# Optimization experiments

Measured on AMD Instinct MI355X. Metric: run time of the kernel, lower is better.

The kernel has to match this reference:

```python
import jax, jax.numpy as jnp
import numpy as np

NUM_VARS = 10
HID = 256
INP = 4
B = 32
T = 64

_adj = np.ones((NUM_VARS, NUM_VARS)) - np.eye(NUM_VARS)
SEND, RECV = np.where(_adj)          # each [E], E = num_vars*(num_vars-1) = 90
E = len(SEND)
_e2n = np.zeros((NUM_VARS, E), dtype=np.float32)
_e2n[RECV, np.arange(E)] = 1.0       # encode_onehot(recv).T -> [num_vars, E]
E2N = jnp.asarray(_e2n)
SEND_J = jnp.asarray(SEND)
RECV_J = jnp.asarray(RECV)


def _mlp_block(x, w1, b1, w2, b2, gamma, beta):
    # RefNRIMLP: elu(fc1) -> (dropout p=0) -> elu(fc2) -> batchnorm over view(-1, H)
    h = jax.nn.elu(x @ w1 + b1)
    h = jax.nn.elu(h @ w2 + b2)
    mu = h.mean(axis=(0, 1, 2), keepdims=True)
    var = h.var(axis=(0, 1, 2), keepdims=True)
    return gamma * (h - mu) * jax.lax.rsqrt(var + 1e-5) + beta


def setup_inputs() -> dict:
    key = jax.random.key(0)
    ks = jax.random.split(key, 12)

    def xavier(k, fi, fo):
        return jax.random.normal(k, (fi, fo), jnp.float32) * np.sqrt(2.0 / (fi + fo))

    d = {
        "x": jax.random.normal(ks[0], (B, T, NUM_VARS, INP), jnp.float32),
        # mlp1: inp -> hid -> hid
        "w1a": xavier(ks[1], INP, HID), "b1a": jnp.full((HID,), 0.1),
        "w1b": xavier(ks[2], HID, HID), "b1b": jnp.full((HID,), 0.1),
        "g1": jnp.ones((HID,)), "be1": jnp.zeros((HID,)),
        # mlp2: 2*hid -> hid -> hid
        "w2a": xavier(ks[3], 2 * HID, HID), "b2a": jnp.full((HID,), 0.1),
        "w2b": xavier(ks[4], HID, HID), "b2b": jnp.full((HID,), 0.1),
        "g2": jnp.ones((HID,)), "be2": jnp.zeros((HID,)),
        # mlp3: hid -> hid -> hid
        "w3a": xavier(ks[5], HID, HID), "b3a": jnp.full((HID,), 0.1),
        "w3b": xavier(ks[6], HID, HID), "b3b": jnp.full((HID,), 0.1),
        "g3": jnp.ones((HID,)), "be3": jnp.zeros((HID,)),
        # output heads
        "wo1": xavier(ks[7], HID, HID), "bo1": jnp.full((HID,), 0.1),
        "wo2": xavier(ks[8], HID, 1), "bo2": jnp.full((1,), 0.1),
    }
    return d


def reference(x, w1a, b1a, w1b, b1b, g1, be1,
              w2a, b2a, w2b, b2b, g2, be2,
              w3a, b3a, w3b, b3b, g3, be3,
              wo1, bo1, wo2, bo2):
    # x: [B, T, N, INP] -> transpose(2,1): [B, N, T, INP]
    h = jnp.transpose(x, (0, 2, 1, 3))
    h = _mlp_block(h, w1a, b1a, w1b, b1b, g1, be1)            # [B, N, T, H]
    # node2edge: gather senders/receivers along node dim, concat on features
    e = jnp.concatenate([h[:, SEND_J], h[:, RECV_J]], axis=-1)  # [B, E, T, 2H]
    e = _mlp_block(e, w2a, b2a, w2b, b2b, g2, be2)            # [B, E, T, H]
    # edge2node: incidence matmul over edge dim, normalize by in-degree
    n = jnp.einsum('ve,betH->bvtH', E2N, e) / (NUM_VARS - 1)   # [B, N, T, H]
    n = _mlp_block(n, w3a, b3a, w3b, b3b, g3, be3)
    n = jax.nn.relu(n) @ wo1 + bo1
    n = jax.nn.relu(n) @ wo2 + bo2                             # [B, N, T, 1]
    out = jnp.transpose(n, (0, 2, 1, 3)).mean(axis=-1)         # [B, T, N]
    return out
```

## Files before the change

kernel.cpp:

```cpp
#include <hip/hip_runtime.h>
#include <hip/hip_bf16.h>
#include <cstdint>

#define DI __device__ __forceinline__

typedef short bf16x8 __attribute__((ext_vector_type(8)));
typedef float f32x4 __attribute__((ext_vector_type(4)));
typedef unsigned short u16;
typedef unsigned short u16x8 __attribute__((ext_vector_type(8)));

static constexpr int NV = 10, NE = 90, TT = 64;
static constexpr int R1 = 20480;
static constexpr int R2 = 184320;

DI float bf2f(u16 u) { union { unsigned int i; float f; } x; x.i = ((unsigned int)u) << 16; return x.f; }
DI u16 f2bf(float f) { unsigned int u = __float_as_uint(f); return (u16)((u + 0x7FFF + ((u >> 16) & 1)) >> 16); }
DI float elu(float v) { return v > 0.f ? v : __expf(v) - 1.f; }

#define GLL(srcp, dstp) __builtin_amdgcn_global_load_lds( \
    (const __attribute__((address_space(1))) unsigned int*)(srcp), \
    (__attribute__((address_space(3))) unsigned int*)(dstp), 16, 0, 0)

__global__ __launch_bounds__(256) void pack5(
    const float* __restrict__ s0, u16* __restrict__ d0,
    const float* __restrict__ s1, u16* __restrict__ d1,
    const float* __restrict__ s2, u16* __restrict__ d2,
    const float* __restrict__ s3, u16* __restrict__ d3,
    const float* __restrict__ s4, u16* __restrict__ d4) {
    const float* s; u16* d;
    switch (blockIdx.y) {
        case 0: s = s0; d = d0; break;
        case 1: s = s1; d = d1; break;
        case 2: s = s2; d = d2; break;
        case 3: s = s3; d = d3; break;
        default: s = s4; d = d4; break;
    }
    int tid = threadIdx.x;
    int bn = blockIdx.x >> 3, kt = blockIdx.x & 7;
#pragma unroll
    for (int p = 0; p < 2; ++p) {
        int n = bn * 128 + p * 64 + (tid >> 2);
        int k = kt * 32 + (tid & 3) * 8;
        u16x8 pk;
#pragma unroll
        for (int e = 0; e < 8; ++e) pk[e] = f2bf(s[(size_t)(k + e) * 256 + n]);
        *(u16x8*)(d + ((size_t)((bn * 8 + kt) * 2 + p)) * 2048 + (size_t)tid * 8) = pk;
    }
}

__global__ __launch_bounds__(256) void pack_w2a(const float* __restrict__ w2a,
                                                const float* __restrict__ scsh1,
                                                u16* __restrict__ d) {
    int tid = threadIdx.x;
    int bn = blockIdx.x >> 4, kt = blockIdx.x & 15;
#pragma unroll
    for (int p = 0; p < 2; ++p) {
        int n = bn * 128 + p * 64 + (tid >> 2);
        int k = kt * 32 + (tid & 3) * 8;
        u16x8 pk;
#pragma unroll
        for (int e = 0; e < 8; ++e)
            pk[e] = f2bf(scsh1[(k + e) & 255] * w2a[(size_t)(k + e) * 256 + n]);
        *(u16x8*)(d + ((size_t)((bn * 16 + kt) * 2 + p)) * 2048 + (size_t)tid * 8) = pk;
    }
}

__global__ void zero_stats(float* p, int n) {
    int i = blockIdx.x * 256 + threadIdx.x;
    if (i < n) p[i] = 0.f;
}

__global__ void conv_wo2(const float* __restrict__ src, u16* __restrict__ dst) {
    dst[threadIdx.x] = f2bf(src[threadIdx.x]);
}

__global__ __launch_bounds__(256) void fold_b2a(const float* __restrict__ w2a,
                                                const float* __restrict__ scsh1,
                                                const float* __restrict__ b2a,
                                                float* __restrict__ b2aF) {
    __shared__ float red[256];
    int n = blockIdx.x, tid = threadIdx.x;
    float sc = scsh1[256 + tid];
    float s = sc * w2a[tid * 256 + n] + sc * w2a[(tid + 256) * 256 + n];
    red[tid] = s;
    __syncthreads();
    for (int off2 = 128; off2 > 0; off2 >>= 1) {
        if (tid < off2) red[tid] += red[tid + off2];
        __syncthreads();
    }
    if (tid == 0) b2aF[n] = red[0] + b2a[n];
}

__global__ void stats_final(const float* __restrict__ sums, const float* __restrict__ g,
                            const float* __restrict__ be, float invR, float* __restrict__ scsh) {
    int c = threadIdx.x;
    float mu = sums[c] * invR;
    float var = sums[256 + c] * invR - mu * mu;
    float rs = rsqrtf(var + 1e-5f);
    float sc = g[c] * rs;
    scsh[c] = sc;
    scsh[256 + c] = be[c] - mu * sc;
}

__global__ __launch_bounds__(256) void mlp1_fc1(const float* __restrict__ x,
                                                const float* __restrict__ w1a,
                                                const float* __restrict__ b1a,
                                                u16* __restrict__ ha) {
    int tid = threadIdx.x;
    int row = blockIdx.x * 8 + (tid >> 5);
    int ch8 = (tid & 31) * 8;
    int b = row / (NV * TT);
    int v = (row >> 6) % NV;
    int t = row & 63;
    const float* xp = x + ((size_t)(b * TT + t) * NV + v) * 4;
    float x0 = xp[0], x1 = xp[1], x2 = xp[2], x3 = xp[3];
    u16x8 pack;
#pragma unroll
    for (int e = 0; e < 8; ++e) {
        int c = ch8 + e;
        float acc = b1a[c] + x0 * w1a[c] + x1 * w1a[256 + c] + x2 * w1a[512 + c] + x3 * w1a[768 + c];
        pack[e] = f2bf(elu(acc));
    }
    *(u16x8*)(ha + (size_t)row * 256 + ch8) = pack;
}

template <bool GATHER, int ACT, bool STATS, int SWZ>
__global__ __launch_bounds__(256) void gemm_kernel(const u16* __restrict__ A,
                                                   const u16* __restrict__ Wt,
                                                   const float* __restrict__ bias,
                                                   u16* __restrict__ out,
                                                   int K,
                                                   float* __restrict__ stats) {
    __shared__ u16 As[3][128 * 32];
    __shared__ u16 Bs[3][128 * 32];
    const int tid = threadIdx.x;
    const int lane = tid & 63, wid = tid >> 6;

    int bm, bn;
    {
        int bid = blockIdx.x;
        int xcd = bid & 7, slot = bid >> 3;
        if constexpr (SWZ == 1) {
            int batch = xcd + 8 * (slot / 90);
            int j = slot % 90;
            bn = j & 1;
            bm = batch * 45 + (j >> 1);
        } else {
            bn = slot & 1;
            bm = xcd + 8 * (slot >> 1);
        }
    }
    const int m0 = bm * 128, n0 = bn * 128;
    const int wm = wid >> 1, wn = wid & 1;

    const int srow = tid >> 2;
    const int scol8 = (tid & 3) * 8;

    size_t abase[2], sb[2], rb[2];
    if constexpr (GATHER) {
#pragma unroll
        for (int p = 0; p < 2; ++p) {
            int m = m0 + srow + p * 64;
            int t = m & 63;
            int be = m >> 6;
            int e = be % NE;
            int b = be / NE;
            int s = e / 9;
            int kk = e - s * 9;
            int r = kk + (kk >= s ? 1 : 0);
            sb[p] = ((size_t)((b * NV + s) * TT + t)) * 256;
            rb[p] = ((size_t)((b * NV + r) * TT + t)) * 256;
        }
    } else {
#pragma unroll
        for (int p = 0; p < 2; ++p) abase[p] = (size_t)(m0 + srow + p * 64) * K;
    }
    const int NT = K >> 5;
    const size_t bnbase = (size_t)bn * NT * 4096;

    f32x4 acc[4][4];
#pragma unroll
    for (int i = 0; i < 4; ++i)
#pragma unroll
        for (int j = 0; j < 4; ++j) acc[i][j] = (f32x4)0.f;

    const int lrow = lane & 15;
    const int lk8 = (lane >> 4) * 8;

    auto stage = [&](int bf, int k0) {
        const size_t btile = bnbase + (size_t)(k0 >> 5) * 4096 + (size_t)tid * 8;
#pragma unroll
        for (int p = 0; p < 2; ++p) {
            const u16* asrc;
            if constexpr (GATHER) {
                int f = k0 + scol8;
                asrc = A + (f < 256 ? sb[p] + f : rb[p] + (f - 256));
            } else {
                asrc = A + abase[p] + k0 + scol8;
            }
            GLL(asrc, &As[bf][(p * 256 + wid * 64) * 8]);
            GLL(Wt + btile + p * 2048, &Bs[bf][(p * 256 + wid * 64) * 8]);
        }
    };

    stage(0, 0);
    stage(1, 32);
    for (int kt = 0; kt < NT; ++kt) {
        if (kt + 1 < NT) {
            asm volatile("s_waitcnt vmcnt(4)" ::: "memory");
        } else {
            asm volatile("s_waitcnt vmcnt(0)" ::: "memory");
        }
        __builtin_amdgcn_s_barrier();
        if (kt + 2 < NT) stage((kt + 2) % 3, (kt + 2) * 32);
        __builtin_amdgcn_sched_barrier(0);
        const int buf = kt % 3;
        bf16x8 a[4], b[4];
#pragma unroll
        for (int i = 0; i < 4; ++i)
            a[i] = *(const bf16x8*)&As[buf][(wm * 64 + i * 16 + lrow) * 32 + lk8];
#pragma unroll
        for (int j = 0; j < 4; ++j)
            b[j] = *(const bf16x8*)&Bs[buf][(wn * 64 + j * 16 + lrow) * 32 + lk8];
#pragma unroll
        for (int i = 0; i < 4; ++i)
#pragma unroll
            for (int j = 0; j < 4; ++j)
                acc[i][j] = __builtin_amdgcn_mfma_f32_16x16x32_bf16(a[i], b[j], acc[i][j], 0, 0, 0);
    }

    float bv[4], sv[4], qv[4];
#pragma unroll
    for (int j = 0; j < 4; ++j) {
        bv[j] = bias[n0 + wn * 64 + j * 16 + lrow];
        if constexpr (STATS) { sv[j] = 0.f; qv[j] = 0.f; }
    }
#pragma unroll
    for (int i = 0; i < 4; ++i) {
#pragma unroll
        for (int j = 0; j < 4; ++j) {
            int col = n0 + wn * 64 + j * 16 + lrow;
#pragma unroll
            for (int r = 0; r < 4; ++r) {
                int row = m0 + wm * 64 + i * 16 + (lane >> 4) * 4 + r;
                float v = acc[i][j][r] + bv[j];
                v = (ACT == 1) ? elu(v) : (v > 0.f ? v : 0.f);
                if constexpr (STATS) { sv[j] += v; qv[j] += v * v; }
                out[(size_t)row * 256 + col] = f2bf(v);
            }
        }
    }
    if constexpr (STATS) {
#pragma unroll
        for (int j = 0; j < 4; ++j) {
            float s = sv[j], q_ = qv[j];
            s += __shfl_xor(s, 16); q_ += __shfl_xor(q_, 16);
            s += __shfl_xor(s, 32); q_ += __shfl_xor(q_, 32);
            if ((lane >> 4) == 0) {
                int col = n0 + wn * 64 + j * 16 + lrow;
                atomicAdd(&stats[col], s);
                atomicAdd(&stats[256 + col], q_);
            }
        }
    }
}

__global__ __launch_bounds__(256) void norm_affine_relu(const u16* __restrict__ in,
                                                        const float* __restrict__ scsh,
                                                        u16* __restrict__ out, int n8) {
    int i = blockIdx.x * 256 + threadIdx.x;
    if (i >= n8) return;
    size_t base = (size_t)i * 8;
    int ch8 = (int)(base & 255);
    u16x8 v = *(const u16x8*)(in + base);
    u16x8 o;
#pragma unroll
    for (int e = 0; e < 8; ++e) {
        float f = bf2f(v[e]);
        f = scsh[ch8 + e] * f + scsh[256 + ch8 + e];
        o[e] = f2bf(f > 0.f ? f : 0.f);
    }
    *(u16x8*)(out + base) = o;
}

__global__ __launch_bounds__(256) void edge2node(const u16* __restrict__ h2,
                                                 const float* __restrict__ scsh2,
                                                 u16* __restrict__ n1) {
    int tid = threadIdx.x;
    int row = blockIdx.x * 8 + (tid >> 5);
    int ch8 = (tid & 31) * 8;
    int t = row & 63;
    int bv = row >> 6;
    int v = bv % NV;
    int b = bv / NV;
    float acc[8] = {0, 0, 0, 0, 0, 0, 0, 0};
#pragma unroll
    for (int i = 0; i < 9; ++i) {
        int s = i + (i >= v ? 1 : 0);
        int e = s * 9 + (v < s ? v : v - 1);
        u16x8 vv = *(const u16x8*)(h2 + ((size_t)((b * NE + e) * TT + t)) * 256 + ch8);
#pragma unroll
        for (int k = 0; k < 8; ++k) acc[k] += bf2f(vv[k]);
    }
    const float inv9 = 1.f / 9.f;
    u16x8 o;
#pragma unroll
    for (int k = 0; k < 8; ++k) {
        int c = ch8 + k;
        o[k] = f2bf(scsh2[c] * (acc[k] * inv9) + scsh2[256 + c]);
    }
    *(u16x8*)(n1 + (size_t)row * 256 + ch8) = o;
}

__global__ __launch_bounds__(256) void head2(const u16* __restrict__ a2,
                                             const u16* __restrict__ wo2t,
                                             const float* __restrict__ bo2,
                                             float* __restrict__ out) {
    int tid = threadIdx.x;
    int row = blockIdx.x * 8 + (tid >> 5);
    int l32 = tid & 31;
    int ch8 = l32 * 8;
    u16x8 a = *(const u16x8*)(a2 + (size_t)row * 256 + ch8);
    u16x8 w = *(const u16x8*)(wo2t + ch8);
    float p = 0.f;
#pragma unroll
    for (int k = 0; k < 8; ++k) p += bf2f(a[k]) * bf2f(w[k]);
#pragma unroll
    for (int off = 16; off > 0; off >>= 1) p += __shfl_down(p, off, 32);
    if (l32 == 0) {
        int b = row / (NV * TT);
        int v = (row >> 6) % NV;
        int t = row & 63;
        out[(size_t)(b * TT + t) * NV + v] = p + bo2[0];
    }
}

extern "C" void kernel_launch(void* const* d_in, const int* in_sizes, int n_in,
                              void* d_out, int out_size, void* d_ws, size_t ws_size,
                              hipStream_t stream) {
    const float* x   = (const float*)d_in[0];
    const float* w1a = (const float*)d_in[1];
    const float* b1a = (const float*)d_in[2];
    const float* w1b = (const float*)d_in[3];
    const float* b1b = (const float*)d_in[4];
    const float* g1  = (const float*)d_in[5];
    const float* be1 = (const float*)d_in[6];
    const float* w2a = (const float*)d_in[7];
    const float* b2a = (const float*)d_in[8];
    const float* w2b = (const float*)d_in[9];
    const float* b2b = (const float*)d_in[10];
    const float* g2  = (const float*)d_in[11];
    const float* be2 = (const float*)d_in[12];
    const float* w3a = (const float*)d_in[13];
    const float* b3a = (const float*)d_in[14];
    const float* w3b = (const float*)d_in[15];
    const float* b3b = (const float*)d_in[16];
    const float* g3  = (const float*)d_in[17];
    const float* be3 = (const float*)d_in[18];
    const float* wo1 = (const float*)d_in[19];
    const float* bo1 = (const float*)d_in[20];
    const float* wo2 = (const float*)d_in[21];
    const float* bo2 = (const float*)d_in[22];
    float* out = (float*)d_out;

    char* ws = (char*)d_ws;
    size_t off = 0;
    auto alloc = [&](size_t bytes) {
        void* p = ws + off;
        off = (off + bytes + 255) & ~(size_t)255;
        return p;
    };
    u16* w1bP = (u16*)alloc(2 * 8 * 4096 * 2);
    u16* w2aP = (u16*)alloc(2 * 16 * 4096 * 2);
    u16* w2bP = (u16*)alloc(2 * 8 * 4096 * 2);
    u16* w3aP = (u16*)alloc(2 * 8 * 4096 * 2);
    u16* w3bP = (u16*)alloc(2 * 8 * 4096 * 2);
    u16* wo1P = (u16*)alloc(2 * 8 * 4096 * 2);
    u16* wo2T = (u16*)alloc(256 * 2);
    float* sums  = (float*)alloc(3 * 512 * 4);
    float* scsh1 = (float*)alloc(512 * 4);
    float* scsh2 = (float*)alloc(512 * 4);
    float* scsh3 = (float*)alloc(512 * 4);
    float* b2aF  = (float*)alloc(256 * 4);
    u16* S0 = (u16*)alloc((size_t)R1 * 256 * 2);
    u16* S1 = (u16*)alloc((size_t)R1 * 256 * 2);
    u16* S2 = (u16*)alloc((size_t)R1 * 256 * 2);
    u16* BIG1 = (u16*)alloc((size_t)R2 * 256 * 2);
    u16* BIG2 = (u16*)alloc((size_t)R2 * 256 * 2);

    dim3 pgrid(16, 5);
    pack5<<<pgrid, 256, 0, stream>>>(w1b, w1bP, w2b, w2bP, w3a, w3aP,
                                     w3b, w3bP, wo1, wo1P);
    zero_stats<<<6, 256, 0, stream>>>(sums, 3 * 512);
    conv_wo2<<<1, 256, 0, stream>>>(wo2, wo2T);

    mlp1_fc1<<<R1 / 8, 256, 0, stream>>>(x, w1a, b1a, S0);
    gemm_kernel<false, 1, true, 0><<<(R1 / 128) * 2, 256, 0, stream>>>(S0, w1bP, b1b, S1, 256, sums);
    stats_final<<<1, 256, 0, stream>>>(sums, g1, be1, 1.f / R1, scsh1);
    pack_w2a<<<32, 256, 0, stream>>>(w2a, scsh1, w2aP);
    fold_b2a<<<256, 256, 0, stream>>>(w2a, scsh1, b2a, b2aF);

    gemm_kernel<true, 1, false, 1><<<(R2 / 128) * 2, 256, 0, stream>>>(S1, w2aP, b2aF, BIG1, 512, nullptr);
    gemm_kernel<false, 1, true, 0><<<(R2 / 128) * 2, 256, 0, stream>>>(BIG1, w2bP, b2b, BIG2, 256, sums + 512);
    stats_final<<<1, 256, 0, stream>>>(sums + 512, g2, be2, 1.f / R2, scsh2);

    edge2node<<<R1 / 8, 256, 0, stream>>>(BIG2, scsh2, S0);

    gemm_kernel<false, 1, false, 0><<<(R1 / 128) * 2, 256, 0, stream>>>(S0, w3aP, b3a, S1, 256, nullptr);
    gemm_kernel<false, 1, true, 0><<<(R1 / 128) * 2, 256, 0, stream>>>(S1, w3bP, b3b, S2, 256, sums + 1024);
    stats_final<<<1, 256, 0, stream>>>(sums + 1024, g3, be3, 1.f / R1, scsh3);

    norm_affine_relu<<<(R1 * 32 + 255) / 256, 256, 0, stream>>>(S2, scsh3, S0, R1 * 32);
    gemm_kernel<false, 2, false, 0><<<(R1 / 128) * 2, 256, 0, stream>>>(S0, wo1P, bo1, S1, 256, nullptr);
    head2<<<R1 / 8, 256, 0, stream>>>(S1, wo2T, bo2, out);
}
```

Before: 260.5 us.

## Use full-width 256x256 tiles with 512 threads for the edge MLP GEMMs

Adds a gemm256 kernel in which each 512-thread block computes a 256-row by full 256-column output tile. It is used for the two large edge-MLP GEMMs (with gather and with stats), and their weights are repacked into a matching full-width layout. This stops the gathered A rows from being loaded twice by the two column-half blocks and halves the number of stats atomics. In exchange each thread holds twice as many accumulators and the block uses more LDS, which can reduce occupancy. The XCD swizzle also changes: each XCD now gets a contiguous range of row tiles.

After: 266.3 us. +2.2%, slower.

```diff
diff --git a/kernel.cpp b/kernel.cpp
--- a/kernel.cpp
+++ b/kernel.cpp
@@ -21,19 +21,17 @@
     (const __attribute__((address_space(1))) unsigned int*)(srcp), \
     (__attribute__((address_space(3))) unsigned int*)(dstp), 16, 0, 0)
 
-__global__ __launch_bounds__(256) void pack5(
+__global__ __launch_bounds__(256) void pack4(
     const float* __restrict__ s0, u16* __restrict__ d0,
     const float* __restrict__ s1, u16* __restrict__ d1,
     const float* __restrict__ s2, u16* __restrict__ d2,
-    const float* __restrict__ s3, u16* __restrict__ d3,
-    const float* __restrict__ s4, u16* __restrict__ d4) {
+    const float* __restrict__ s3, u16* __restrict__ d3) {
     const float* s; u16* d;
     switch (blockIdx.y) {
         case 0: s = s0; d = d0; break;
         case 1: s = s1; d = d1; break;
         case 2: s = s2; d = d2; break;
-        case 3: s = s3; d = d3; break;
-        default: s = s4; d = d4; break;
+        default: s = s3; d = d3; break;
     }
     int tid = threadIdx.x;
     int bn = blockIdx.x >> 3, kt = blockIdx.x & 7;
@@ -48,20 +46,41 @@
     }
 }
 
-__global__ __launch_bounds__(256) void pack_w2a(const float* __restrict__ w2a,
-                                                const float* __restrict__ scsh1,
-                                                u16* __restrict__ d) {
-    int tid = threadIdx.x;
-    int bn = blockIdx.x >> 4, kt = blockIdx.x & 15;
-#pragma unroll
-    for (int p = 0; p < 2; ++p) {
-        int n = bn * 128 + p * 64 + (tid >> 2);
-        int k = kt * 32 + (tid & 3) * 8;
-        u16x8 pk;
-#pragma unroll
-        for (int e = 0; e < 8; ++e)
-            pk[e] = f2bf(scsh1[(k + e) & 255] * w2a[(size_t)(k + e) * 256 + n]);
-        *(u16x8*)(d + ((size_t)((bn * 16 + kt) * 2 + p)) * 2048 + (size_t)tid * 8) = pk;
+__global__ __launch_bounds__(256) void pack256(const float* __restrict__ s,
+                                               u16* __restrict__ d) {
+    int kt = blockIdx.x;
+#pragma unroll
+    for (int h = 0; h < 2; ++h) {
+        int tid2 = threadIdx.x + h * 256;
+#pragma unroll
+        for (int p = 0; p < 2; ++p) {
+            int n = p * 128 + (tid2 >> 2);
+            int k = kt * 32 + (tid2 & 3) * 8;
+            u16x8 pk;
+#pragma unroll
+            for (int e = 0; e < 8; ++e) pk[e] = f2bf(s[(size_t)(k + e) * 256 + n]);
+            *(u16x8*)(d + ((size_t)(kt * 2 + p)) * 4096 + (size_t)tid2 * 8) = pk;
+        }
+    }
+}
+
+__global__ __launch_bounds__(256) void pack256_w2a(const float* __restrict__ w2a,
+                                                   const float* __restrict__ scsh1,
+                                                   u16* __restrict__ d) {
+    int kt = blockIdx.x;
+#pragma unroll
+    for (int h = 0; h < 2; ++h) {
+        int tid2 = threadIdx.x + h * 256;
+#pragma unroll
+        for (int p = 0; p < 2; ++p) {
+            int n = p * 128 + (tid2 >> 2);
+            int k = kt * 32 + (tid2 & 3) * 8;
+            u16x8 pk;
+#pragma unroll
+            for (int e = 0; e < 8; ++e)
+                pk[e] = f2bf(scsh1[(k + e) & 255] * w2a[(size_t)(k + e) * 256 + n]);
+            *(u16x8*)(d + ((size_t)(kt * 2 + p)) * 4096 + (size_t)tid2 * 8) = pk;
+        }
     }
 }
 
@@ -124,7 +143,7 @@
     *(u16x8*)(ha + (size_t)row * 256 + ch8) = pack;
 }
 
-template <bool GATHER, int ACT, bool STATS, int SWZ>
+template <int ACT, bool STATS>
 __global__ __launch_bounds__(256) void gemm_kernel(const u16* __restrict__ A,
                                                    const u16* __restrict__ Wt,
                                                    const float* __restrict__ bias,
@@ -140,15 +159,8 @@
     {
         int bid = blockIdx.x;
         int xcd = bid & 7, slot = bid >> 3;
-        if constexpr (SWZ == 1) {
-            int batch = xcd + 8 * (slot / 90);
-            int j = slot % 90;
-            bn = j & 1;
-            bm = batch * 45 + (j >> 1);
-        } else {
-            bn = slot & 1;
-            bm = xcd + 8 * (slot >> 1);
-        }
+        bn = slot & 1;
+        bm = xcd + 8 * (slot >> 1);
     }
     const int m0 = bm * 128, n0 = bn * 128;
     const int wm = wid >> 1, wn = wid & 1;
@@ -156,25 +168,8 @@
     const int srow = tid >> 2;
     const int scol8 = (tid & 3) * 8;
 
-    size_t abase[2], sb[2], rb[2];
-    if constexpr (GATHER) {
-#pragma unroll
-        for (int p = 0; p < 2; ++p) {
-            int m = m0 + srow + p * 64;
-            int t = m & 63;
-            int be = m >> 6;
-            int e = be % NE;
-            int b = be / NE;
-            int s = e / 9;
-            int kk = e - s * 9;
-            int r = kk + (kk >= s ? 1 : 0);
-            sb[p] = ((size_t)((b * NV + s) * TT + t)) * 256;
-            rb[p] = ((size_t)((b * NV + r) * TT + t)) * 256;
-        }
-    } else {
-#pragma unroll
-        for (int p = 0; p < 2; ++p) abase[p] = (size_t)(m0 + srow + p * 64) * K;
-    }
+    size_t abase0 = (size_t)(m0 + srow) * K;
+    size_t abase1 = (size_t)(m0 + srow + 64) * K;
     const int NT = K >> 5;
     const size_t bnbase = (size_t)bn * NT * 4096;
 
@@ -189,18 +184,10 @@
 
     auto stage = [&](int bf, int k0) {
         const size_t btile = bnbase + (size_t)(k0 >> 5) * 4096 + (size_t)tid * 8;
-#pragma unroll
-        for (int p = 0; p < 2; ++p) {
-            const u16* asrc;
-            if constexpr (GATHER) {
-                int f = k0 + scol8;
-                asrc = A + (f < 256 ? sb[p] + f : rb[p] + (f - 256));
-            } else {
-                asrc = A + abase[p] + k0 + scol8;
-            }
-            GLL(asrc, &As[bf][(p * 256 + wid * 64) * 8]);
-            GLL(Wt + btile + p * 2048, &Bs[bf][(p * 256 + wid * 64) * 8]);
-        }
+        GLL(A + abase0 + k0 + scol8, &As[bf][(wid * 64) * 8]);
+        GLL(Wt + btile, &Bs[bf][(wid * 64) * 8]);
+        GLL(A + abase1 + k0 + scol8, &As[bf][(256 + wid * 64) * 8]);
+        GLL(Wt + btile + 2048, &Bs[bf][(256 + wid * 64) * 8]);
     };
 
     stage(0, 0);
@@ -258,6 +245,135 @@
             s += __shfl_xor(s, 32); q_ += __shfl_xor(q_, 32);
             if ((lane >> 4) == 0) {
                 int col = n0 + wn * 64 + j * 16 + lrow;
+                atomicAdd(&stats[col], s);
+                atomicAdd(&stats[256 + col], q_);
+            }
+        }
+    }
+}
+
+template <bool GATHER, bool STATS>
+__global__ __launch_bounds__(512) void gemm256(const u16* __restrict__ A,
+                                               const u16* __restrict__ PK,
+                                               const float* __restrict__ bias,
+                                               u16* __restrict__ out,
+                                               int K,
+                                               float* __restrict__ stats) {
+    __shared__ u16 As[3][256 * 32];
+    __shared__ u16 Bs[3][256 * 32];
+    const int tid = threadIdx.x;
+    const int lane = tid & 63, wid = tid >> 6;
+
+    const int bm = (blockIdx.x & 7) * 90 + (blockIdx.x >> 3);
+    const int m0 = bm * 256;
+    const int wm = wid >> 2, wn = wid & 3;
+
+    const int srow = tid >> 2;
+    const int scol8 = (tid & 3) * 8;
+
+    size_t ab0 = 0, ab1 = 0, sb0 = 0, sb1 = 0, rb0 = 0, rb1 = 0;
+    if constexpr (GATHER) {
+        {
+            int m = m0 + srow;
+            int t = m & 63, be = m >> 6, e = be % NE, b = be / NE;
+            int s = e / 9, kk = e - s * 9, r = kk + (kk >= s ? 1 : 0);
+            sb0 = ((size_t)((b * NV + s) * TT + t)) * 256;
+            rb0 = ((size_t)((b * NV + r) * TT + t)) * 256;
+        }
+        {
+            int m = m0 + srow + 128;
+            int t = m & 63, be = m >> 6, e = be % NE, b = be / NE;
+            int s = e / 9, kk = e - s * 9, r = kk + (kk >= s ? 1 : 0);
+            sb1 = ((size_t)((b * NV + s) * TT + t)) * 256;
+            rb1 = ((size_t)((b * NV + r) * TT + t)) * 256;
+        }
+    } else {
+        ab0 = (size_t)(m0 + srow) * K;
+        ab1 = (size_t)(m0 + srow + 128) * K;
+    }
+    const int NT = K >> 5;
+
+    f32x4 acc[8][4];
+#pragma unroll
+    for (int i = 0; i < 8; ++i)
+#pragma unroll
+        for (int j = 0; j < 4; ++j) acc[i][j] = (f32x4)0.f;
+
+    const int lrow = lane & 15;
+    const int lk8 = (lane >> 4) * 8;
+
+    auto stage = [&](int bf, int k0) {
+        const size_t btile = (size_t)(k0 >> 5) * 8192 + (size_t)tid * 8;
+        const u16 *a0, *a1;
+        if constexpr (GATHER) {
+            int f = k0 + scol8;
+            a0 = A + (f < 256 ? sb0 + f : rb0 + (f - 256));
+            a1 = A + (f < 256 ? sb1 + f : rb1 + (f - 256));
+        } else {
+            a0 = A + ab0 + k0 + scol8;
+            a1 = A + ab1 + k0 + scol8;
+        }
+        GLL(a0, &As[bf][tid * 8]);
+        GLL(PK + btile, &Bs[bf][tid * 8]);
+        GLL(a1, &As[bf][4096 + tid * 8]);
+        GLL(PK + btile + 4096, &Bs[bf][4096 + tid * 8]);
+    };
+
+    stage(0, 0);
+    stage(1, 32);
+    for (int kt = 0; kt < NT; ++kt) {
+        if (kt + 1 < NT) {
+            asm volatile("s_waitcnt vmcnt(4)" ::: "memory");
+        } else {
+            asm volatile("s_waitcnt vmcnt(0)" ::: "memory");
+        }
+        __builtin_amdgcn_s_barrier();
+        if (kt + 2 < NT) stage((kt + 2) % 3, (kt + 2) * 32);
+        __builtin_amdgcn_sched_barrier(0);
+        const int buf = kt % 3;
+        bf16x8 a[8], b[4];
+#pragma unroll
+        for (int i = 0; i < 8; ++i)
+            a[i] = *(const bf16x8*)&As[buf][(wm * 128 + i * 16 + lrow) * 32 + lk8];
+#pragma unroll
+        for (int j = 0; j < 4; ++j)
+            b[j] = *(const bf16x8*)&Bs[buf][(wn * 64 + j * 16 + lrow) * 32 + lk8];
+#pragma unroll
+        for (int i = 0; i < 8; ++i)
+#pragma unroll
+            for (int j = 0; j < 4; ++j)
+                acc[i][j] = __builtin_amdgcn_mfma_f32_16x16x32_bf16(a[i], b[j], acc[i][j], 0, 0, 0);
+    }
+
+    float bv[4], sv[4], qv[4];
+#pragma unroll
+    for (int j = 0; j < 4; ++j) {
+        bv[j] = bias[wn * 64 + j * 16 + lrow];
+        if constexpr (STATS) { sv[j] = 0.f; qv[j] = 0.f; }
+    }
+#pragma unroll
+    for (int i = 0; i < 8; ++i) {
+#pragma unroll
+        for (int j = 0; j < 4; ++j) {
+            int col = wn * 64 + j * 16 + lrow;
+#pragma unroll
+            for (int r = 0; r < 4; ++r) {
+                int row = m0 + wm * 128 + i * 16 + (lane >> 4) * 4 + r;
+                float v = acc[i][j][r] + bv[j];
+                v = elu(v);
+                if constexpr (STATS) { sv[j] += v; qv[j] += v * v; }
+                out[(size_t)row * 256 + col] = f2bf(v);
+            }
+        }
+    }
+    if constexpr (STATS) {
+#pragma unroll
+        for (int j = 0; j < 4; ++j) {
+            float s = sv[j], q_ = qv[j];
+            s += __shfl_xor(s, 16); q_ += __shfl_xor(q_, 16);
+            s += __shfl_xor(s, 32); q_ += __shfl_xor(q_, 32);
+            if ((lane >> 4) == 0) {
+                int col = wn * 64 + j * 16 + lrow;
                 atomicAdd(&stats[col], s);
                 atomicAdd(&stats[256 + col], q_);
             }
@@ -371,11 +487,11 @@
         return p;
     };
     u16* w1bP = (u16*)alloc(2 * 8 * 4096 * 2);
-    u16* w2aP = (u16*)alloc(2 * 16 * 4096 * 2);
-    u16* w2bP = (u16*)alloc(2 * 8 * 4096 * 2);
     u16* w3aP = (u16*)alloc(2 * 8 * 4096 * 2);
     u16* w3bP = (u16*)alloc(2 * 8 * 4096 * 2);
     u16* wo1P = (u16*)alloc(2 * 8 * 4096 * 2);
+    u16* w2aP = (u16*)alloc(16 * 8192 * 2);
+    u16* w2bP = (u16*)alloc(8 * 8192 * 2);
     u16* wo2T = (u16*)alloc(256 * 2);
     float* sums  = (float*)alloc(3 * 512 * 4);
     float* scsh1 = (float*)alloc(512 * 4);
@@ -388,29 +504,29 @@
     u16* BIG1 = (u16*)alloc((size_t)R2 * 256 * 2);
     u16* BIG2 = (u16*)alloc((size_t)R2 * 256 * 2);
 
-    dim3 pgrid(16, 5);
-    pack5<<<pgrid, 256, 0, stream>>>(w1b, w1bP, w2b, w2bP, w3a, w3aP,
-                                     w3b, w3bP, wo1, wo1P);
+    dim3 pgrid(16, 4);
+    pack4<<<pgrid, 256, 0, stream>>>(w1b, w1bP, w3a, w3aP, w3b, w3bP, wo1, wo1P);
+    pack256<<<8, 256, 0, stream>>>(w2b, w2bP);
     zero_stats<<<6, 256, 0, stream>>>(sums, 3 * 512);
     conv_wo2<<<1, 256, 0, stream>>>(wo2, wo2T);
 
     mlp1_fc1<<<R1 / 8, 256, 0, stream>>>(x, w1a, b1a, S0);
-    gemm_kernel<false, 1, true, 0><<<(R1 / 128) * 2, 256, 0, stream>>>(S0, w1bP, b1b, S1, 256, sums);
+    gemm_kernel<1, true><<<(R1 / 128) * 2, 256, 0, stream>>>(S0, w1bP, b1b, S1, 256, sums);
     stats_final<<<1, 256, 0, stream>>>(sums, g1, be1, 1.f / R1, scsh1);
-    pack_w2a<<<32, 256, 0, stream>>>(w2a, scsh1, w2aP);
+    pack256_w2a<<<16, 256, 0, stream>>>(w2a, scsh1, w2aP);
     fold_b2a<<<256, 256, 0, stream>>>(w2a, scsh1, b2a, b2aF);
 
-    gemm_kernel<true, 1, false, 1><<<(R2 / 128) * 2, 256, 0, stream>>>(S1, w2aP, b2aF, BIG1, 512, nullptr);
-    gemm_kernel<false, 1, true, 0><<<(R2 / 128) * 2, 256, 0, stream>>>(BIG1, w2bP, b2b, BIG2, 256, sums + 512);
+    gemm256<true, false><<<R2 / 256, 512, 0, stream>>>(S1, w2aP, b2aF, BIG1, 512, nullptr);
+    gemm256<false, true><<<R2 / 256, 512, 0, stream>>>(BIG1, w2bP, b2b, BIG2, 256, sums + 512);
     stats_final<<<1, 256, 0, stream>>>(sums + 512, g2, be2, 1.f / R2, scsh2);
 
     edge2node<<<R1 / 8, 256, 0, stream>>>(BIG2, scsh2, S0);
 
-    gemm_kernel<false, 1, false, 0><<<(R1 / 128) * 2, 256, 0, stream>>>(S0, w3aP, b3a, S1, 256, nullptr);
-    gemm_kernel<false, 1, true, 0><<<(R1 / 128) * 2, 256, 0, stream>>>(S1, w3bP, b3b, S2, 256, sums + 1024);
+    gemm_kernel<1, false><<<(R1 / 128) * 2, 256, 0, stream>>>(S0, w3aP, b3a, S1, 256, nullptr);
+    gemm_kernel<1, true><<<(R1 / 128) * 2, 256, 0, stream>>>(S1, w3bP, b3b, S2, 256, sums + 1024);
     stats_final<<<1, 256, 0, stream>>>(sums + 1024, g3, be3, 1.f / R1, scsh3);
 
     norm_affine_relu<<<(R1 * 32 + 255) / 256, 256, 0, stream>>>(S2, scsh3, S0, R1 * 32);
-    gemm_kernel<false, 2, false, 0><<<(R1 / 128) * 2, 256, 0, stream>>>(S0, wo1P, bo1, S1, 256, nullptr);
+    gemm_kernel<2, false><<<(R1 / 128) * 2, 256, 0, stream>>>(S0, wo1P, bo1, S1, 256, nullptr);
     head2<<<R1 / 8, 256, 0, stream>>>(S1, wo2T, bo2, out);
 }
```
